# Kernel optimization log

Measured on AMD Instinct MI355X. Metric: run time of the kernel, lower is better.

## Reference

```python
import jax, jax.numpy as jnp
import numpy as np
import math

B, S, H, DK = 16, 4096, 16, 64
DM = H * DK          # 1024, d_model
QD = 1024            # q_d_model
KVD = 1024           # kv_d_model
MASK_P = 0.85        # randbool probability


def setup_inputs() -> dict:
    key = jax.random.key(0)
    ks = jax.random.split(key, 12)
    s = 0.02
    return {
        "q": jax.random.normal(ks[0], (B, 1, QD), jnp.float32),
        "k": jax.random.normal(ks[1], (B, S, KVD), jnp.float32),
        "v": jax.random.normal(ks[2], (B, S, KVD), jnp.float32),
        "Wq": jax.random.normal(ks[3], (QD, DM), jnp.float32) * s,
        "bq": jnp.zeros((DM,), jnp.float32),
        "Wk": jax.random.normal(ks[4], (KVD, DM), jnp.float32) * s,
        "bk": jnp.zeros((DM,), jnp.float32),
        "Wv": jax.random.normal(ks[5], (KVD, DM), jnp.float32) * s,
        "bv": jnp.zeros((DM,), jnp.float32),
        "Wo": jax.random.normal(ks[6], (DM, QD), jnp.float32) * s,
        "bo": jnp.zeros((QD,), jnp.float32),
        # randbool(shape, p=0.85): True where rand < p -> score zeroed
        "maskfill": jax.random.uniform(ks[7], (B, H, 1, S)) < MASK_P,
    }


def reference(q, k, v, Wq, bq, Wk, bk, Wv, bv, Wo, bo, maskfill):
    bs = q.shape[0]
    # projections -> [B, L, H, DK] -> [B, H, L, DK]
    qh = (q @ Wq + bq).reshape(bs, -1, H, DK).transpose(0, 2, 1, 3)  # [B,H,1,DK]
    kh = (k @ Wk + bk).reshape(bs, -1, H, DK).transpose(0, 2, 1, 3)  # [B,H,S,DK]
    vh = (v @ Wv + bv).reshape(bs, -1, H, DK).transpose(0, 2, 1, 3)  # [B,H,S,DK]

    scores1 = jnp.einsum("bhqd,bhkd->bhqk", qh, kh) / math.sqrt(DK)  # [B,H,1,S]

    # plain path (dropout = identity in eval)
    attn = jax.nn.softmax(scores1, axis=-1)
    out_h = jnp.einsum("bhqk,bhkd->bhqd", attn, vh)                  # [B,H,1,DK]

    # masked path: zero-fill (not -inf) masked raw scores, then softmax
    masked_scores = jnp.where(maskfill, 0.0, scores1)
    mattn = jax.nn.softmax(masked_scores, axis=-1)
    mout_h = jnp.einsum("bhqk,bhkd->bhqd", mattn, vh)

    concat = out_h.transpose(0, 2, 1, 3).reshape(bs, DM)
    mconcat = mout_h.transpose(0, 2, 1, 3).reshape(bs, DM)
    output = concat @ Wo + bo
    masked_output = mconcat @ Wo + bo
    return (output, masked_output)
```

## Files before the change

kernel.cpp:

```cpp
#include <hip/hip_runtime.h>
#include <stdint.h>

#define NB 16
#define NS 4096
#define NH 16
#define NC 1024

#define OFF_QHP   0u
#define OFF_QK    262144u
#define OFF_QB    524288u
#define OFF_FLAG  524544u
#define OFF_SP    524608u
#define OFF_S     557376u
#define OFF_ATT   557888u
#define OFF_CTXP  2655040u
#define OFF_CTX   11043648u
#define OFF_CON   11567936u

__global__ void k_maskprobe(const uint32_t* __restrict__ m, int* __restrict__ flag) {
    __shared__ int sf, sg;
    if (threadIdx.x == 0) { sf = 0; sg = 0; }
    __syncthreads();
    uint32_t x = m[threadIdx.x];
    if (x == 0x3F800000u) atomicOr(&sf, 1);
    else if (x > 1u) atomicOr(&sg, 1);
    __syncthreads();
    if (threadIdx.x == 0) *flag = sf ? 2 : (sg ? 1 : 0);
}

__global__ __launch_bounds__(128) void k_qh(
    const float* __restrict__ q, const float* __restrict__ Wq, float* __restrict__ qhp)
{
    __shared__ float qs[64*16];
    int dz = blockIdx.x, cs = blockIdx.y;
    int tid = threadIdx.x;
    int d = dz*128 + tid;
#pragma unroll
    for (int j = 0; j < 2; ++j) {
        int idx = j*128 + tid;
        int b = idx >> 4, c4 = (idx & 15) << 2;
        float4 t = *(const float4*)(q + (size_t)b*NC + cs*64 + c4);
        qs[(c4+0)*16 + b] = t.x; qs[(c4+1)*16 + b] = t.y;
        qs[(c4+2)*16 + b] = t.z; qs[(c4+3)*16 + b] = t.w;
    }
    __syncthreads();
    float acc[16];
#pragma unroll
    for (int b = 0; b < 16; ++b) acc[b] = 0.f;
#pragma unroll 4
    for (int c = 0; c < 64; ++c) {
        float w = Wq[(size_t)(cs*64 + c)*NC + d];
        const float4* qr = (const float4*)(qs + c*16);
        float4 q0 = qr[0], q1 = qr[1], q2 = qr[2], q3 = qr[3];
        acc[0]  = fmaf(w, q0.x, acc[0]);  acc[1]  = fmaf(w, q0.y, acc[1]);
        acc[2]  = fmaf(w, q0.z, acc[2]);  acc[3]  = fmaf(w, q0.w, acc[3]);
        acc[4]  = fmaf(w, q1.x, acc[4]);  acc[5]  = fmaf(w, q1.y, acc[5]);
        acc[6]  = fmaf(w, q1.z, acc[6]);  acc[7]  = fmaf(w, q1.w, acc[7]);
        acc[8]  = fmaf(w, q2.x, acc[8]);  acc[9]  = fmaf(w, q2.y, acc[9]);
        acc[10] = fmaf(w, q2.z, acc[10]); acc[11] = fmaf(w, q2.w, acc[11]);
        acc[12] = fmaf(w, q3.x, acc[12]); acc[13] = fmaf(w, q3.y, acc[13]);
        acc[14] = fmaf(w, q3.z, acc[14]); acc[15] = fmaf(w, q3.w, acc[15]);
    }
#pragma unroll
    for (int b = 0; b < 16; ++b) qhp[((size_t)cs*16 + b)*NC + d] = acc[b];
}

__global__ __launch_bounds__(128) void k_qk(
    const float* __restrict__ qhp, const float* __restrict__ bq,
    const float* __restrict__ Wk, const float* __restrict__ bk,
    float* __restrict__ qko, float* __restrict__ qbv)
{
    int h = blockIdx.x;
    int c = blockIdx.y*128 + threadIdx.x;
    __shared__ float qs[16*64];
    for (int j = 0; j < 8; ++j) {
        int idx = j*128 + threadIdx.x;
        int b = idx >> 6, dd = idx & 63;
        float a = bq[h*64 + dd];
#pragma unroll
        for (int cs = 0; cs < 16; ++cs) a += qhp[((size_t)cs*16 + b)*NC + h*64 + dd];
        qs[idx] = a;
    }
    __syncthreads();
    const float* wr = Wk + (size_t)c*NC + h*64;
    float acc[16];
#pragma unroll
    for (int b = 0; b < 16; ++b) acc[b] = 0.f;
#pragma unroll 4
    for (int d = 0; d < 64; ++d) {
        float w = wr[d];
#pragma unroll
        for (int b = 0; b < 16; ++b) acc[b] = fmaf(qs[b*64 + d], w, acc[b]);
    }
#pragma unroll
    for (int b = 0; b < 16; ++b) qko[((size_t)b*NH + h)*NC + c] = acc[b];
    if (blockIdx.y == 0 && threadIdx.x < 16) {
        int b = threadIdx.x; float a = 0.f;
        for (int d = 0; d < 64; ++d) a = fmaf(qs[b*64 + d], bk[h*64 + d], a);
        qbv[b*NH + h] = a;
    }
}

#define QTS 20
__global__ __launch_bounds__(256) void k_scoresG2(
    const float* __restrict__ kk, const float* __restrict__ qkm,
    const float* __restrict__ qbv, const void* __restrict__ mask,
    const int* __restrict__ flagp, float* __restrict__ att, float* __restrict__ Sp)
{
    __shared__ float qt[256*QTS];
    __shared__ float red[4][2][16];
    int sb = blockIdx.x, b = blockIdx.y;
    int tid = threadIdx.x;
    int g = tid >> 2, ph = tid & 3;
    int s = sb*64 + g;
    const float* kbase = kk + ((size_t)b*NS + s)*NC + ph*4;
    float acc[16];
#pragma unroll
    for (int h = 0; h < 16; ++h) acc[h] = 0.f;

    for (int cz = 0; cz < 4; ++cz) {
        __syncthreads();
#pragma unroll
        for (int j = 0; j < 16; ++j) {
            int idx = j*256 + tid;
            int h = idx >> 8, c = idx & 255;
            qt[c*QTS + h] = qkm[((size_t)b*NH + h)*NC + cz*256 + c];
        }
        __syncthreads();
#pragma unroll
        for (int w = 0; w < 16; ++w) {
            float4 kv = *(const float4*)(kbase + cz*256 + w*16);
#pragma unroll
            for (int j = 0; j < 4; ++j) {
                float kc = (j == 0) ? kv.x : (j == 1) ? kv.y : (j == 2) ? kv.z : kv.w;
                const float* qp = qt + (w*16 + ph*4 + j)*QTS;
                float4 q0 = *(const float4*)(qp + 0);
                float4 q1 = *(const float4*)(qp + 4);
                float4 q2 = *(const float4*)(qp + 8);
                float4 q3 = *(const float4*)(qp + 12);
                acc[0]  = fmaf(kc, q0.x, acc[0]);
                acc[1]  = fmaf(kc, q0.y, acc[1]);
                acc[2]  = fmaf(kc, q0.z, acc[2]);
                acc[3]  = fmaf(kc, q0.w, acc[3]);
                acc[4]  = fmaf(kc, q1.x, acc[4]);
                acc[5]  = fmaf(kc, q1.y, acc[5]);
                acc[6]  = fmaf(kc, q1.z, acc[6]);
                acc[7]  = fmaf(kc, q1.w, acc[7]);
                acc[8]  = fmaf(kc, q2.x, acc[8]);
                acc[9]  = fmaf(kc, q2.y, acc[9]);
                acc[10] = fmaf(kc, q2.z, acc[10]);
                acc[11] = fmaf(kc, q2.w, acc[11]);
                acc[12] = fmaf(kc, q3.x, acc[12]);
                acc[13] = fmaf(kc, q3.y, acc[13]);
                acc[14] = fmaf(kc, q3.z, acc[14]);
                acc[15] = fmaf(kc, q3.w, acc[15]);
            }
        }
    }
#pragma unroll
    for (int h = 0; h < 16; ++h) {
        acc[h] += __shfl_xor(acc[h], 1, 64);
        acc[h] += __shfl_xor(acc[h], 2, 64);
    }

    int h0 = ph*4;
    int fl = *flagp;
    unsigned mbits = 0;
    if (fl == 1) {
        const uint8_t* mp = (const uint8_t*)mask + (size_t)(b*NH + h0)*NS + s;
#pragma unroll
        for (int j = 0; j < 4; ++j) if (mp[(size_t)j*NS]) mbits |= (1u << j);
    } else if (fl == 2) {
        const float* mp = (const float*)mask + (size_t)(b*NH + h0)*NS + s;
#pragma unroll
        for (int j = 0; j < 4; ++j) if (mp[(size_t)j*NS] != 0.f) mbits |= (1u << j);
    } else {
        const int* mp = (const int*)mask + (size_t)(b*NH + h0)*NS + s;
#pragma unroll
        for (int j = 0; j < 4; ++j) if (mp[(size_t)j*NS]) mbits |= (1u << j);
    }
    float p0[4], p1[4], r0[4], r1[4];
#pragma unroll
    for (int j = 0; j < 4; ++j) {
        float val = (acc[h0+j] + qbv[b*NH + h0 + j]) * 0.125f;
        p0[j] = __expf(val);
        p1[j] = (mbits >> j & 1u) ? 1.0f : p0[j];
        r0[j] = p0[j]; r1[j] = p1[j];
    }
    float* arow = att + ((size_t)b*NS + s)*32;
    *(float4*)(arow + h0)      = make_float4(p0[0], p0[1], p0[2], p0[3]);
    *(float4*)(arow + 16 + h0) = make_float4(p1[0], p1[1], p1[2], p1[3]);

#pragma unroll
    for (int off = 4; off < 64; off <<= 1)
#pragma unroll
        for (int j = 0; j < 4; ++j) {
            r0[j] += __shfl_xor(r0[j], off, 64);
            r1[j] += __shfl_xor(r1[j], off, 64);
        }
    int wv = tid >> 6;
    if ((tid & 63) < 4) {
#pragma unroll
        for (int j = 0; j < 4; ++j) {
            red[wv][0][(tid & 3)*4 + j] = r0[j];
            red[wv][1][(tid & 3)*4 + j] = r1[j];
        }
    }
    __syncthreads();
    if (tid < 32) {
        int pa = tid >> 4, h = tid & 15;
        Sp[((size_t)b*64 + sb)*32 + tid] =
            red[0][pa][h] + red[1][pa][h] + red[2][pa][h] + red[3][pa][h];
    }
}

__global__ void k_sred(const float* __restrict__ Sp, float* __restrict__ S) {
    int t = blockIdx.x*256 + threadIdx.x;
    int p = t >> 8, b = (t >> 4) & 15, h = t & 15;
    float a = 0.f;
#pragma unroll
    for (int sb = 0; sb < 64; ++sb) a += Sp[((size_t)b*64 + sb)*32 + p*16 + h];
    S[t] = a;
}

__global__ __launch_bounds__(256,2) void k_ctx(
    const float* __restrict__ v, const float* __restrict__ att, float* __restrict__ ctxp)
{
    __shared__ float al[64*32];
    __shared__ float buf[8192];
    int b = blockIdx.x & 15, ss = blockIdx.x >> 4;
    int cz = blockIdx.y;
    int tid = threadIdx.x, ct = tid & 63, rg = tid >> 6;
    int s1 = ss * 256;
    float acc[32][4];
#pragma unroll
    for (int i = 0; i < 32; ++i)
#pragma unroll
        for (int j = 0; j < 4; ++j) acc[i][j] = 0.f;

    for (int c0 = 0; c0 < 256; c0 += 64) {
        __syncthreads();
#pragma unroll
        for (int jj = 0; jj < 2; ++jj) {
            int idx = jj*256 + tid;
            ((float4*)al)[idx] = ((const float4*)(att + ((size_t)b*NS + s1 + c0)*32))[idx];
        }
        __syncthreads();
        for (int it = 0; it < 16; ++it) {
            int rl = c0 + it*4 + rg;
            float4 vv = *(const float4*)(v + ((size_t)b*NS + s1 + rl)*NC + cz*256 + ct*4);
            const float4* ar = (const float4*)(al + (it*4 + rg)*32);
#pragma unroll
            for (int u = 0; u < 8; ++u) {
                float4 aw = ar[u];
                acc[u*4+0][0] = fmaf(aw.x, vv.x, acc[u*4+0][0]);
                acc[u*4+0][1] = fmaf(aw.x, vv.y, acc[u*4+0][1]);
                acc[u*4+0][2] = fmaf(aw.x, vv.z, acc[u*4+0][2]);
                acc[u*4+0][3] = fmaf(aw.x, vv.w, acc[u*4+0][3]);
                acc[u*4+1][0] = fmaf(aw.y, vv.x, acc[u*4+1][0]);
                acc[u*4+1][1] = fmaf(aw.y, vv.y, acc[u*4+1][1]);
                acc[u*4+1][2] = fmaf(aw.y, vv.z, acc[u*4+1][2]);
                acc[u*4+1][3] = fmaf(aw.y, vv.w, acc[u*4+1][3]);
                acc[u*4+2][0] = fmaf(aw.z, vv.x, acc[u*4+2][0]);
                acc[u*4+2][1] = fmaf(aw.z, vv.y, acc[u*4+2][1]);
                acc[u*4+2][2] = fmaf(aw.z, vv.z, acc[u*4+2][2]);
                acc[u*4+2][3] = fmaf(aw.z, vv.w, acc[u*4+2][3]);
                acc[u*4+3][0] = fmaf(aw.w, vv.x, acc[u*4+3][0]);
                acc[u*4+3][1] = fmaf(aw.w, vv.y, acc[u*4+3][1]);
                acc[u*4+3][2] = fmaf(aw.w, vv.z, acc[u*4+3][2]);
                acc[u*4+3][3] = fmaf(aw.w, vv.w, acc[u*4+3][3]);
            }
        }
    }
    for (int pr = 0; pr < 4; ++pr) {
        __syncthreads();
#pragma unroll
        for (int u = 0; u < 8; ++u) {
            int ph = pr*8 + u;
            float4 t; t.x = acc[ph][0]; t.y = acc[ph][1]; t.z = acc[ph][2]; t.w = acc[ph][3];
            ((float4*)buf)[(rg*8 + u)*64 + ct] = t;
        }
        __syncthreads();
#pragma unroll
        for (int kx = 0; kx < 2; ++kx) {
            int i = kx*256 + tid;
            int u2 = i >> 6, c2 = i & 63;
            float4 s = ((float4*)buf)[(size_t)(0*8 + u2)*64 + c2];
#pragma unroll
            for (int r2 = 1; r2 < 4; ++r2) {
                float4 t = ((float4*)buf)[(size_t)(r2*8 + u2)*64 + c2];
                s.x += t.x; s.y += t.y; s.z += t.z; s.w += t.w;
            }
            int ph = pr*8 + u2, p = ph >> 4, h = ph & 15;
            *(float4*)(ctxp + ((((size_t)ss*2 + p)*NB + b)*NH + h)*NC + cz*256 + c2*4) = s;
        }
    }
}

__global__ void k_ctxred(const float* __restrict__ ctxp, const float* __restrict__ S,
                         float* __restrict__ ctx) {
    size_t i = (size_t)blockIdx.x * 256 + threadIdx.x;
    float a = 0.f;
#pragma unroll
    for (int ss = 0; ss < 16; ++ss) a += ctxp[(size_t)ss*524288 + i];
    ctx[i] = a / S[i >> 10];
}

__global__ __launch_bounds__(256) void k_outh(
    const float* __restrict__ ctx, const float* __restrict__ Wv,
    const float* __restrict__ bv, float* __restrict__ con)
{
    int b = blockIdx.y, p = blockIdx.z;
    int d = blockIdx.x*256 + threadIdx.x;
    int h0 = blockIdx.x*4;
    __shared__ float cl[4*NC];
    for (int i = threadIdx.x; i < 4*NC; i += 256)
        cl[i] = ctx[(((size_t)p*NB + b)*NH + h0 + (i >> 10))*NC + (i & 1023)];
    __syncthreads();
    const float* c2 = cl + ((threadIdx.x >> 6) << 10);
    float a0=0.f,a1=0.f,a2=0.f,a3=0.f;
    for (int c = 0; c < NC; c += 4) {
        a0 = fmaf(c2[c+0], Wv[(size_t)(c+0)*NC + d], a0);
        a1 = fmaf(c2[c+1], Wv[(size_t)(c+1)*NC + d], a1);
        a2 = fmaf(c2[c+2], Wv[(size_t)(c+2)*NC + d], a2);
        a3 = fmaf(c2[c+3], Wv[(size_t)(c+3)*NC + d], a3);
    }
    con[((size_t)p*NB + b)*NC + d] = (a0+a1)+(a2+a3) + bv[d];
}

__global__ __launch_bounds__(256) void k_out(
    const float* __restrict__ con, const float* __restrict__ Wo,
    const float* __restrict__ bo, float* __restrict__ out)
{
    int b = blockIdx.y, p = blockIdx.z;
    int o = blockIdx.x*256 + threadIdx.x;
    __shared__ float cl[NC];
    for (int i = threadIdx.x; i < NC; i += 256)
        cl[i] = con[((size_t)p*NB + b)*NC + i];
    __syncthreads();
    float a0=0.f,a1=0.f,a2=0.f,a3=0.f;
    for (int m = 0; m < NC; m += 4) {
        a0 = fmaf(cl[m+0], Wo[(size_t)(m+0)*NC + o], a0);
        a1 = fmaf(cl[m+1], Wo[(size_t)(m+1)*NC + o], a1);
        a2 = fmaf(cl[m+2], Wo[(size_t)(m+2)*NC + o], a2);
        a3 = fmaf(cl[m+3], Wo[(size_t)(m+3)*NC + o], a3);
    }
    out[(size_t)p*NB*NC + (size_t)b*NC + o] = (a0+a1)+(a2+a3) + bo[o];
}

extern "C" void kernel_launch(void* const* d_in, const int* in_sizes, int n_in,
                              void* d_out, int out_size, void* d_ws, size_t ws_size,
                              hipStream_t stream)
{
    (void)in_sizes; (void)n_in; (void)out_size; (void)ws_size;
    const float* q  = (const float*)d_in[0];
    const float* k  = (const float*)d_in[1];
    const float* v  = (const float*)d_in[2];
    const float* Wq = (const float*)d_in[3];
    const float* bq = (const float*)d_in[4];
    const float* Wk = (const float*)d_in[5];
    const float* bk = (const float*)d_in[6];
    const float* Wv = (const float*)d_in[7];
    const float* bv = (const float*)d_in[8];
    const float* Wo = (const float*)d_in[9];
    const float* bo = (const float*)d_in[10];
    const void*  mk = d_in[11];

    float* ws   = (float*)d_ws;
    float* qhp  = ws + OFF_QHP;
    float* qkv  = ws + OFF_QK;
    float* qbv  = ws + OFF_QB;
    int*   flg  = (int*)(ws + OFF_FLAG);
    float* Sp   = ws + OFF_SP;
    float* S    = ws + OFF_S;
    float* att  = ws + OFF_ATT;
    float* ctxp = ws + OFF_CTXP;
    float* ctx  = ws + OFF_CTX;
    float* con  = ws + OFF_CON;
    float* out  = (float*)d_out;

    k_maskprobe<<<1, 1024, 0, stream>>>((const uint32_t*)mk, flg);
    k_qh<<<dim3(8, 16), 128, 0, stream>>>(q, Wq, qhp);
    k_qk<<<dim3(16, 8), 128, 0, stream>>>(qhp, bq, Wk, bk, qkv, qbv);
    k_scoresG2<<<dim3(64, 16), 256, 0, stream>>>(k, qkv, qbv, mk, flg, att, Sp);
    k_sred<<<2, 256, 0, stream>>>(Sp, S);
    k_ctx<<<dim3(256, 4), 256, 0, stream>>>(v, att, ctxp);
    k_ctxred<<<2048, 256, 0, stream>>>(ctxp, S, ctx);
    k_outh<<<dim3(4, NB, 2), 256, 0, stream>>>(ctx, Wv, bv, con);
    k_out<<<dim3(4, NB, 2), 256, 0, stream>>>(con, Wo, bo, out);
}
```

Measured before the change: 307.3 us.

## Retile scores kernel to 8 rows x 4 heads per thread with prefetch

Restructures the K·(Wk q) scores kernel so each thread accumulates 8 sequence rows by 4 heads instead of 1 row by 16 heads. This cuts LDS reads of the q tile per FMA, and K loads for the next column chunk are software-prefetched into registers. Blocks now cover 128 rows with a 512-column LDS tile, which halves the grid and the partial-sum count consumed by k_sred. The cost is more registers, possibly lower occupancy, and only 512 blocks in flight.

```diff
diff --git a/kernel.cpp b/kernel.cpp
--- a/kernel.cpp
+++ b/kernel.cpp
@@ -102,114 +102,144 @@
 }
 
 #define QTS 20
-__global__ __launch_bounds__(256) void k_scoresG2(
+__global__ __launch_bounds__(256) void k_scoresI(
     const float* __restrict__ kk, const float* __restrict__ qkm,
     const float* __restrict__ qbv, const void* __restrict__ mask,
     const int* __restrict__ flagp, float* __restrict__ att, float* __restrict__ Sp)
 {
-    __shared__ float qt[256*QTS];
+    __shared__ float qt[512*QTS];
     __shared__ float red[4][2][16];
     int sb = blockIdx.x, b = blockIdx.y;
     int tid = threadIdx.x;
-    int g = tid >> 2, ph = tid & 3;
-    int s = sb*64 + g;
-    const float* kbase = kk + ((size_t)b*NS + s)*NC + ph*4;
-    float acc[16];
-#pragma unroll
-    for (int h = 0; h < 16; ++h) acc[h] = 0.f;
-
-    for (int cz = 0; cz < 4; ++cz) {
-        __syncthreads();
-#pragma unroll
-        for (int j = 0; j < 16; ++j) {
+    int ph = tid & 3, hg = (tid >> 2) & 3, rg = tid >> 4;
+    int srow = sb*128 + rg*8;
+    const float* kr = kk + ((size_t)b*NS + srow)*NC + ph*4;
+    float acc[8][4];
+#pragma unroll
+    for (int i = 0; i < 8; ++i)
+#pragma unroll
+        for (int j = 0; j < 4; ++j) acc[i][j] = 0.f;
+
+    for (int cz = 0; cz < 2; ++cz) {
+        __syncthreads();
+#pragma unroll
+        for (int j = 0; j < 32; ++j) {
             int idx = j*256 + tid;
-            int h = idx >> 8, c = idx & 255;
-            qt[c*QTS + h] = qkm[((size_t)b*NH + h)*NC + cz*256 + c];
-        }
-        __syncthreads();
-#pragma unroll
-        for (int w = 0; w < 16; ++w) {
-            float4 kv = *(const float4*)(kbase + cz*256 + w*16);
+            int h = idx >> 9, c = idx & 511;
+            qt[c*QTS + h] = qkm[((size_t)b*NH + h)*NC + cz*512 + c];
+        }
+        __syncthreads();
+        const float* kc0 = kr + cz*512;
+        float4 kv[8], kn[8];
+#pragma unroll
+        for (int i = 0; i < 8; ++i) kv[i] = *(const float4*)(kc0 + i*NC);
+        for (int w = 0; w < 32; ++w) {
+            if (w < 31) {
+#pragma unroll
+                for (int i = 0; i < 8; ++i)
+                    kn[i] = *(const float4*)(kc0 + i*NC + (w+1)*16);
+            }
 #pragma unroll
             for (int j = 0; j < 4; ++j) {
-                float kc = (j == 0) ? kv.x : (j == 1) ? kv.y : (j == 2) ? kv.z : kv.w;
-                const float* qp = qt + (w*16 + ph*4 + j)*QTS;
-                float4 q0 = *(const float4*)(qp + 0);
-                float4 q1 = *(const float4*)(qp + 4);
-                float4 q2 = *(const float4*)(qp + 8);
-                float4 q3 = *(const float4*)(qp + 12);
-                acc[0]  = fmaf(kc, q0.x, acc[0]);
-                acc[1]  = fmaf(kc, q0.y, acc[1]);
-                acc[2]  = fmaf(kc, q0.z, acc[2]);
-                acc[3]  = fmaf(kc, q0.w, acc[3]);
-                acc[4]  = fmaf(kc, q1.x, acc[4]);
-                acc[5]  = fmaf(kc, q1.y, acc[5]);
-                acc[6]  = fmaf(kc, q1.z, acc[6]);
-                acc[7]  = fmaf(kc, q1.w, acc[7]);
-                acc[8]  = fmaf(kc, q2.x, acc[8]);
-                acc[9]  = fmaf(kc, q2.y, acc[9]);
-                acc[10] = fmaf(kc, q2.z, acc[10]);
-                acc[11] = fmaf(kc, q2.w, acc[11]);
-                acc[12] = fmaf(kc, q3.x, acc[12]);
-                acc[13] = fmaf(kc, q3.y, acc[13]);
-                acc[14] = fmaf(kc, q3.z, acc[14]);
-                acc[15] = fmaf(kc, q3.w, acc[15]);
+                const float* qp = qt + (w*16 + ph*4 + j)*QTS + hg*4;
+                float4 qv = *(const float4*)qp;
+#pragma unroll
+                for (int i = 0; i < 8; ++i) {
+                    float kc = (j == 0) ? kv[i].x : (j == 1) ? kv[i].y
+                             : (j == 2) ? kv[i].z : kv[i].w;
+                    acc[i][0] = fmaf(kc, qv.x, acc[i][0]);
+                    acc[i][1] = fmaf(kc, qv.y, acc[i][1]);
+                    acc[i][2] = fmaf(kc, qv.z, acc[i][2]);
+                    acc[i][3] = fmaf(kc, qv.w, acc[i][3]);
+                }
             }
-        }
-    }
-#pragma unroll
-    for (int h = 0; h < 16; ++h) {
-        acc[h] += __shfl_xor(acc[h], 1, 64);
-        acc[h] += __shfl_xor(acc[h], 2, 64);
-    }
-
-    int h0 = ph*4;
+#pragma unroll
+            for (int i = 0; i < 8; ++i) kv[i] = kn[i];
+        }
+    }
+#pragma unroll
+    for (int i = 0; i < 8; ++i)
+#pragma unroll
+        for (int j = 0; j < 4; ++j) {
+            acc[i][j] += __shfl_xor(acc[i][j], 1, 64);
+            acc[i][j] += __shfl_xor(acc[i][j], 2, 64);
+        }
+    float d0[4], d1[4];
+    if (ph == 0) {
+#pragma unroll
+        for (int j = 0; j < 4; ++j) { d0[j] = acc[0][j]; d1[j] = acc[1][j]; }
+    } else if (ph == 1) {
+#pragma unroll
+        for (int j = 0; j < 4; ++j) { d0[j] = acc[2][j]; d1[j] = acc[3][j]; }
+    } else if (ph == 2) {
+#pragma unroll
+        for (int j = 0; j < 4; ++j) { d0[j] = acc[4][j]; d1[j] = acc[5][j]; }
+    } else {
+#pragma unroll
+        for (int j = 0; j < 4; ++j) { d0[j] = acc[6][j]; d1[j] = acc[7][j]; }
+    }
+    int sA = srow + 2*ph, sB = sA + 1;
     int fl = *flagp;
-    unsigned mbits = 0;
+    unsigned mA = 0, mB = 0;
     if (fl == 1) {
-        const uint8_t* mp = (const uint8_t*)mask + (size_t)(b*NH + h0)*NS + s;
-#pragma unroll
-        for (int j = 0; j < 4; ++j) if (mp[(size_t)j*NS]) mbits |= (1u << j);
+        const uint8_t* mp = (const uint8_t*)mask + (size_t)(b*NH + hg*4)*NS;
+#pragma unroll
+        for (int j = 0; j < 4; ++j) {
+            if (mp[(size_t)j*NS + sA]) mA |= (1u << j);
+            if (mp[(size_t)j*NS + sB]) mB |= (1u << j);
+        }
     } else if (fl == 2) {
-        const float* mp = (const float*)mask + (size_t)(b*NH + h0)*NS + s;
-#pragma unroll
-        for (int j = 0; j < 4; ++j) if (mp[(size_t)j*NS] != 0.f) mbits |= (1u << j);
+        const float* mp = (const float*)mask + (size_t)(b*NH + hg*4)*NS;
+#pragma unroll
+        for (int j = 0; j < 4; ++j) {
+            if (mp[(size_t)j*NS + sA] != 0.f) mA |= (1u << j);
+            if (mp[(size_t)j*NS + sB] != 0.f) mB |= (1u << j);
+        }
     } else {
-        const int* mp = (const int*)mask + (size_t)(b*NH + h0)*NS + s;
-#pragma unroll
-        for (int j = 0; j < 4; ++j) if (mp[(size_t)j*NS]) mbits |= (1u << j);
-    }
-    float p0[4], p1[4], r0[4], r1[4];
+        const int* mp = (const int*)mask + (size_t)(b*NH + hg*4)*NS;
+#pragma unroll
+        for (int j = 0; j < 4; ++j) {
+            if (mp[(size_t)j*NS + sA]) mA |= (1u << j);
+            if (mp[(size_t)j*NS + sB]) mB |= (1u << j);
+        }
+    }
+    float p0a[4], p1a[4], p0b[4], p1b[4], r0[4], r1[4];
 #pragma unroll
     for (int j = 0; j < 4; ++j) {
-        float val = (acc[h0+j] + qbv[b*NH + h0 + j]) * 0.125f;
-        p0[j] = __expf(val);
-        p1[j] = (mbits >> j & 1u) ? 1.0f : p0[j];
-        r0[j] = p0[j]; r1[j] = p1[j];
-    }
-    float* arow = att + ((size_t)b*NS + s)*32;
-    *(float4*)(arow + h0)      = make_float4(p0[0], p0[1], p0[2], p0[3]);
-    *(float4*)(arow + 16 + h0) = make_float4(p1[0], p1[1], p1[2], p1[3]);
-
-#pragma unroll
-    for (int off = 4; off < 64; off <<= 1)
+        float qb = qbv[b*NH + hg*4 + j];
+        float va = (d0[j] + qb) * 0.125f;
+        float vb = (d1[j] + qb) * 0.125f;
+        p0a[j] = __expf(va);  p1a[j] = (mA >> j & 1u) ? 1.0f : p0a[j];
+        p0b[j] = __expf(vb);  p1b[j] = (mB >> j & 1u) ? 1.0f : p0b[j];
+        r0[j] = p0a[j] + p0b[j];
+        r1[j] = p1a[j] + p1b[j];
+    }
+    float* aA = att + ((size_t)b*NS + sA)*32 + hg*4;
+    float* aB = att + ((size_t)b*NS + sB)*32 + hg*4;
+    *(float4*)(aA)      = make_float4(p0a[0], p0a[1], p0a[2], p0a[3]);
+    *(float4*)(aA + 16) = make_float4(p1a[0], p1a[1], p1a[2], p1a[3]);
+    *(float4*)(aB)      = make_float4(p0b[0], p0b[1], p0b[2], p0b[3]);
+    *(float4*)(aB + 16) = make_float4(p1b[0], p1b[1], p1b[2], p1b[3]);
+
+#pragma unroll
+    for (int j = 0; j < 4; ++j) {
+        r0[j] += __shfl_xor(r0[j], 1, 64);  r1[j] += __shfl_xor(r1[j], 1, 64);
+        r0[j] += __shfl_xor(r0[j], 2, 64);  r1[j] += __shfl_xor(r1[j], 2, 64);
+        r0[j] += __shfl_xor(r0[j], 16, 64); r1[j] += __shfl_xor(r1[j], 16, 64);
+        r0[j] += __shfl_xor(r0[j], 32, 64); r1[j] += __shfl_xor(r1[j], 32, 64);
+    }
+    int wv = tid >> 6;
+    if ((tid & 51) == 0) {
 #pragma unroll
         for (int j = 0; j < 4; ++j) {
-            r0[j] += __shfl_xor(r0[j], off, 64);
-            r1[j] += __shfl_xor(r1[j], off, 64);
-        }
-    int wv = tid >> 6;
-    if ((tid & 63) < 4) {
-#pragma unroll
-        for (int j = 0; j < 4; ++j) {
-            red[wv][0][(tid & 3)*4 + j] = r0[j];
-            red[wv][1][(tid & 3)*4 + j] = r1[j];
+            red[wv][0][hg*4 + j] = r0[j];
+            red[wv][1][hg*4 + j] = r1[j];
         }
     }
     __syncthreads();
     if (tid < 32) {
         int pa = tid >> 4, h = tid & 15;
-        Sp[((size_t)b*64 + sb)*32 + tid] =
+        Sp[((size_t)b*32 + sb)*32 + tid] =
             red[0][pa][h] + red[1][pa][h] + red[2][pa][h] + red[3][pa][h];
     }
 }
@@ -219,7 +249,7 @@
     int p = t >> 8, b = (t >> 4) & 15, h = t & 15;
     float a = 0.f;
 #pragma unroll
-    for (int sb = 0; sb < 64; ++sb) a += Sp[((size_t)b*64 + sb)*32 + p*16 + h];
+    for (int sb = 0; sb < 32; ++sb) a += Sp[((size_t)b*32 + sb)*32 + p*16 + h];
     S[t] = a;
 }
 
@@ -382,7 +412,7 @@
     k_maskprobe<<<1, 1024, 0, stream>>>((const uint32_t*)mk, flg);
     k_qh<<<dim3(8, 16), 128, 0, stream>>>(q, Wq, qhp);
     k_qk<<<dim3(16, 8), 128, 0, stream>>>(qhp, bq, Wk, bk, qkv, qbv);
-    k_scoresG2<<<dim3(64, 16), 256, 0, stream>>>(k, qkv, qbv, mk, flg, att, Sp);
+    k_scoresI<<<dim3(32, 16), 256, 0, stream>>>(k, qkv, qbv, mk, flg, att, Sp);
     k_sred<<<2, 256, 0, stream>>>(Sp, S);
     k_ctx<<<dim3(256, 4), 256, 0, stream>>>(v, att, ctxp);
     k_ctxred<<<2048, 256, 0, stream>>>(ctxp, S, ctx);
```

After: 311.3 us. No clear change (+1.3%).
